# Performance work log

Measured on AMD Instinct MI355X. Metric: run time of the kernel, lower is better.

The kernel has to match this reference:

```python
import jax, jax.numpy as jnp
import numpy as np

P = 8  # patch_size
MD = 32  # metric_dim


def setup_inputs() -> dict:
    key = jax.random.key(0)
    ks = jax.random.split(key, 7)
    b, c, H, W = 4, 3, 512, 512
    s = 1.0 / np.sqrt(MD)
    return {
        "x": jax.random.normal(ks[0], (b, c, H, W), dtype=jnp.float32),
        "conv_w": jax.random.normal(ks[1], (MD, c, P, P), dtype=jnp.float32) * (1.0 / np.sqrt(c * P * P)),
        "conv_b": jax.random.normal(ks[2], (MD,), dtype=jnp.float32) * 0.02,
        "proj_w": jax.random.normal(ks[3], (3 * MD, MD), dtype=jnp.float32) * s,
        "proj_b": jax.random.normal(ks[4], (3 * MD,), dtype=jnp.float32) * 0.02,
        "deconv_w": jax.random.normal(ks[5], (MD, 3, P, P), dtype=jnp.float32) * s,
        "deconv_b": jax.random.normal(ks[6], (3,), dtype=jnp.float32) * 0.02,
    }


def reference(x, conv_w, conv_b, proj_w, proj_b, deconv_w, deconv_b):
    b, c, H, W = x.shape
    hh, ww = H // P, W // P
    # patch embed: Conv2d(kernel=stride=P) == block-reshape + einsum
    xp = x.reshape(b, c, hh, P, ww, P)
    tok = jnp.einsum('bchpwq,ocpq->bohw', xp, conv_w) + conv_b[None, :, None, None]
    # 'b c h w -> b (h w) c'
    tok = tok.reshape(b, MD, hh * ww).transpose(0, 2, 1)  # [b, N, MD]
    xs = tok @ proj_w.T + proj_b
    q, k, v = jnp.split(xs, 3, axis=-1)
    # full NxN QK^T with zeroed diagonal
    lp = jnp.einsum('bnd,bmd->bnm', q, k)
    n = lp.shape[-1]
    i = jnp.arange(n)
    lp = lp.at[:, i, i].set(0.0)
    # cos-phase interference, then matmul with V
    inter = jnp.cos((2.0 * jnp.pi) * lp) @ v  # [b, N, MD]
    # 'b (h w) c -> b c h w'
    inter = inter.transpose(0, 2, 1).reshape(b, MD, hh, ww)
    # ConvTranspose2d(kernel=stride=P) == einsum + block-unreshape
    out = jnp.einsum('bihw,iopq->bohpwq', inter, deconv_w).reshape(b, deconv_w.shape[1], H, W)
    out = out + deconv_b[None, :, None, None]
    return out
```

## Files before the change

### kernel.cpp

```cpp
#include <hip/hip_runtime.h>
#include <hip/hip_bf16.h>

#define NTOK   4096
#define NBATCH 4
#define SPLIT  8

typedef short bf16x8 __attribute__((ext_vector_type(8)));
typedef float f32x4  __attribute__((ext_vector_type(4)));

static __device__ inline short f2bf(float x) {
    __hip_bfloat16 h = __float2bfloat16(x);
    return __builtin_bit_cast(short, h);
}
static __device__ inline float bf2f(short s) {
    return __bfloat162float(__builtin_bit_cast(__hip_bfloat16, s));
}
static __device__ inline f32x4 mfma16(bf16x8 a, bf16x8 b, f32x4 c) {
    return __builtin_amdgcn_mfma_f32_16x16x32_bf16(a, b, c, 0, 0, 0);
}

__global__ __launch_bounds__(512) void k_embed(
    const float* __restrict__ x,  const float* __restrict__ cw,
    const float* __restrict__ cb, const float* __restrict__ pw,
    const float* __restrict__ pb,
    short* __restrict__ qh, short* __restrict__ ql,
    short* __restrict__ kh, short* __restrict__ kl,
    float* __restrict__ vv, float* __restrict__ coef)
{
    __shared__ float tok_lds[64][33];
    __shared__ float qk_lds[64][65];
    const int tid  = threadIdx.x;
    const int og   = tid >> 6;
    const int tl   = tid & 63;
    const int bx   = blockIdx.x;
    const int b    = bx >> 6;
    const int hrow = bx & 63;
    const int n    = hrow * 64 + tl;

    float acc[4];
#pragma unroll
    for (int i = 0; i < 4; ++i) acc[i] = cb[og * 4 + i];

    const float* xb = x + (size_t)b * 3 * 512 * 512;
#pragma unroll
    for (int c = 0; c < 3; ++c) {
        float4 xr[16];
#pragma unroll
        for (int p = 0; p < 8; ++p) {
            const float* row = xb + ((size_t)c * 512 + hrow * 8 + p) * 512 + tl * 8;
            xr[p * 2]     = *(const float4*)row;
            xr[p * 2 + 1] = *(const float4*)(row + 4);
        }
#pragma unroll
        for (int oo = 0; oo < 4; ++oo) {
            const float* wrow = cw + ((size_t)(og * 4 + oo) * 3 + c) * 64;
            float s = 0.f;
#pragma unroll
            for (int j = 0; j < 16; ++j) {
                float4 wv = *(const float4*)(wrow + j * 4);
                s += xr[j].x * wv.x + xr[j].y * wv.y + xr[j].z * wv.z + xr[j].w * wv.w;
            }
            acc[oo] += s;
        }
    }
#pragma unroll
    for (int oo = 0; oo < 4; ++oo) tok_lds[tl][og * 4 + oo] = acc[oo];
    __syncthreads();
    float tok[32];
#pragma unroll
    for (int d = 0; d < 32; ++d) tok[d] = tok_lds[tl][d];

    const int toff = (b * NTOK + n) * 32;
    const int nch  = n >> 4, r16n = n & 15;
#pragma unroll
    for (int g2 = 0; g2 < 3; ++g2) {
        int jb = og * 12 + g2 * 4;
        float r[4];
#pragma unroll
        for (int l2 = 0; l2 < 4; ++l2) {
            int j = jb + l2;
            float s = pb[j];
            const float* prow = pw + j * 32;
#pragma unroll
            for (int d4 = 0; d4 < 8; ++d4) {
                float4 wv = *(const float4*)(prow + d4 * 4);
                s += tok[d4 * 4 + 0] * wv.x + tok[d4 * 4 + 1] * wv.y
                   + tok[d4 * 4 + 2] * wv.z + tok[d4 * 4 + 3] * wv.w;
            }
            r[l2] = s;
        }
        if (jb < 64) {
#pragma unroll
            for (int l2 = 0; l2 < 4; ++l2) qk_lds[tl][jb + l2] = r[l2];
            short hs[4], ls2[4];
#pragma unroll
            for (int l2 = 0; l2 < 4; ++l2) {
                hs[l2]  = f2bf(r[l2]);
                ls2[l2] = f2bf(r[l2] - bf2f(hs[l2]));
            }
            int off = (jb < 32) ? jb : (jb - 32);
            short* dh = (jb < 32) ? qh : kh;
            short* dl = (jb < 32) ? ql : kl;
            size_t pa = ((size_t)(b * 256 + nch) * 64 + ((off >> 3) << 4) + r16n) * 8
                        + (off & 7);
            *(short4*)(dh + pa) = make_short4(hs[0], hs[1], hs[2], hs[3]);
            *(short4*)(dl + pa) = make_short4(ls2[0], ls2[1], ls2[2], ls2[3]);
        } else {
            *(float4*)(vv + toff + (jb - 64)) = make_float4(r[0], r[1], r[2], r[3]);
        }
    }
    __syncthreads();
    if (og == 0) {
        float dp = 0.f;
#pragma unroll
        for (int d = 0; d < 32; ++d) dp += qk_lds[tl][d] * qk_lds[tl][32 + d];
        coef[b * NTOK + n] = 1.f - __builtin_amdgcn_cosf(dp - floorf(dp));
    }
}

__global__ __launch_bounds__(256) void k_varr(
    const float* __restrict__ vv, short* __restrict__ varr)
{
    __shared__ short lds[2048];
    const int tid = threadIdx.x;
    const int bx  = blockIdx.x;
    const int b   = bx >> 7, c = bx & 127;
    const float* vb = vv + ((size_t)b * NTOK + c * 32) * 32;

    const int m  = tid >> 3;
    const int d0 = (tid & 7) * 4;
    float4 v4 = *(const float4*)(vb + tid * 4);
    float vd[4] = {v4.x, v4.y, v4.z, v4.w};
#pragma unroll
    for (int l2 = 0; l2 < 4; ++l2) {
        int d = d0 + l2;
        int dt = d >> 4, r16 = d & 15;
        int g, j;
        if (m < 16) { g = m >> 2; j = m & 3; }
        else        { g = (m - 16) >> 2; j = 4 + ((m - 16) & 3); }
        int lane = g * 16 + r16;
        short hv = f2bf(vd[l2]);
        short lv = f2bf(vd[l2] - bf2f(hv));
        lds[dt * 1024 + 0 * 512 + lane * 8 + j] = hv;
        lds[dt * 1024 + 1 * 512 + lane * 8 + j] = lv;
    }
    __syncthreads();
    *(bf16x8*)(varr + ((size_t)b * 128 + c) * 2048 + tid * 8)
        = *(const bf16x8*)(lds + tid * 8);
}

__global__ __launch_bounds__(256, 3) void k_attn(
    const short* __restrict__ qh, const short* __restrict__ ql,
    const short* __restrict__ kh, const short* __restrict__ kl,
    const short* __restrict__ varr, float* __restrict__ part)
{
    __shared__ float st[128][36];
    const int t = threadIdx.x, l = t & 63, w = t >> 6;
    const int g = l >> 4, r16 = l & 15;
    const int bx = blockIdx.x;
    const int s = bx & 7, b = (bx >> 3) & 3, nb = bx >> 5;
    const int n0 = nb * 128 + w * 32;

    bf16x8 qfh[2], qfl[2];
#pragma unroll
    for (int nt = 0; nt < 2; ++nt) {
        size_t ro = ((size_t)(b * 256 + (n0 >> 4) + nt) * 64 + l) * 8;
        qfh[nt] = *(const bf16x8*)(qh + ro);
        qfl[nt] = *(const bf16x8*)(ql + ro);
    }
    f32x4 acc[2][2];
#pragma unroll
    for (int nt = 0; nt < 2; ++nt)
#pragma unroll
        for (int dt = 0; dt < 2; ++dt)
            acc[nt][dt] = (f32x4){0.f, 0.f, 0.f, 0.f};

    for (int ch = 0; ch < 16; ++ch) {
        const int mc = s * 512 + ch * 32;
        bf16x8 kfh[2], kfl[2];
#pragma unroll
        for (int mh = 0; mh < 2; ++mh) {
            size_t ro = ((size_t)(b * 256 + (mc >> 4) + mh) * 64 + l) * 8;
            kfh[mh] = *(const bf16x8*)(kh + ro);
            kfl[mh] = *(const bf16x8*)(kl + ro);
        }
        const short* vbase = varr + ((size_t)(b * 128 + (mc >> 5))) * 2048;
        bf16x8 vf00 = *(const bf16x8*)(vbase + l * 8);
        bf16x8 vf01 = *(const bf16x8*)(vbase + 512 + l * 8);
        bf16x8 vf10 = *(const bf16x8*)(vbase + 1024 + l * 8);
        bf16x8 vf11 = *(const bf16x8*)(vbase + 1536 + l * 8);

        bf16x8 pah[2], pal[2];
#pragma unroll
        for (int nt = 0; nt < 2; ++nt) {
            f32x4 sa = (f32x4){0.f, 0.f, 0.f, 0.f};
            f32x4 sb = (f32x4){0.f, 0.f, 0.f, 0.f};
            sa = mfma16(kfh[0], qfh[nt], sa);
            sa = mfma16(kfh[0], qfl[nt], sa);
            sa = mfma16(kfl[0], qfh[nt], sa);
            sb = mfma16(kfh[1], qfh[nt], sb);
            sb = mfma16(kfh[1], qfl[nt], sb);
            sb = mfma16(kfl[1], qfh[nt], sb);
#pragma unroll
            for (int r = 0; r < 4; ++r) {
                float xa = sa[r];
                float ca = __builtin_amdgcn_cosf(xa - floorf(xa));
                short ha = f2bf(ca);
                pah[nt][r] = ha;
                pal[nt][r] = f2bf(ca - bf2f(ha));
                float xb2 = sb[r];
                float cb2 = __builtin_amdgcn_cosf(xb2 - floorf(xb2));
                short hb = f2bf(cb2);
                pah[nt][r + 4] = hb;
                pal[nt][r + 4] = f2bf(cb2 - bf2f(hb));
            }
        }
#pragma unroll
        for (int nt = 0; nt < 2; ++nt) {
            acc[nt][0] = mfma16(pah[nt], vf00, acc[nt][0]);
            acc[nt][0] = mfma16(pah[nt], vf01, acc[nt][0]);
            acc[nt][0] = mfma16(pal[nt], vf00, acc[nt][0]);
            acc[nt][1] = mfma16(pah[nt], vf10, acc[nt][1]);
            acc[nt][1] = mfma16(pah[nt], vf11, acc[nt][1]);
            acc[nt][1] = mfma16(pal[nt], vf10, acc[nt][1]);
        }
    }
#pragma unroll
    for (int nt = 0; nt < 2; ++nt)
#pragma unroll
        for (int dt = 0; dt < 2; ++dt)
#pragma unroll
            for (int r = 0; r < 4; ++r)
                st[w * 32 + nt * 16 + 4 * g + r][dt * 16 + r16] = acc[nt][dt][r];
    __syncthreads();
    const int tk = t >> 1, d0 = (t & 1) * 16;
    float* pbp = part + ((size_t)(s * NBATCH + b) * NTOK + nb * 128 + tk) * 32 + d0;
    const float* sp = &st[tk][d0];
#pragma unroll
    for (int q4 = 0; q4 < 4; ++q4)
        *(float4*)(pbp + q4 * 4) = *(const float4*)(sp + q4 * 4);
}

__global__ __launch_bounds__(256) void k_reduce(
    const float* __restrict__ part, const float* __restrict__ vv,
    const float* __restrict__ coef, float* __restrict__ inter)
{
    const int idx = blockIdx.x * 256 + threadIdx.x;
    const int g = idx >> 3, d4 = idx & 7;
    const float* p0 = part + (size_t)g * 32 + d4 * 4;
    float4 s = make_float4(0.f, 0.f, 0.f, 0.f);
#pragma unroll
    for (int sp = 0; sp < SPLIT; ++sp) {
        float4 t = *(const float4*)(p0 + (size_t)sp * (NBATCH * NTOK * 32));
        s.x += t.x; s.y += t.y; s.z += t.z; s.w += t.w;
    }
    const float cf = coef[g];
    float4 v4 = *(const float4*)(vv + (size_t)g * 32 + d4 * 4);
    s.x += cf * v4.x; s.y += cf * v4.y; s.z += cf * v4.z; s.w += cf * v4.w;
    *(float4*)(inter + (size_t)g * 32 + d4 * 4) = s;
}

__global__ __launch_bounds__(512) void k_deconv(
    const float* __restrict__ inter, const float* __restrict__ dw,
    const float* __restrict__ db, float* __restrict__ out)
{
    const int tid  = threadIdx.x;
    const int wv   = tid >> 6;
    const int lane = tid & 63;
    const int bx   = blockIdx.x;
    const int b    = bx >> 6;
    const int hrow = bx & 63;
    const int n    = hrow * 64 + lane;

    float ir[32];
    const float* ip = inter + ((size_t)(b * NTOK + n)) * 32;
#pragma unroll
    for (int d4 = 0; d4 < 8; ++d4) {
        float4 t4 = *(const float4*)(ip + d4 * 4);
        ir[d4 * 4 + 0] = t4.x; ir[d4 * 4 + 1] = t4.y;
        ir[d4 * 4 + 2] = t4.z; ir[d4 * 4 + 3] = t4.w;
    }
#pragma unroll
    for (int rr = 0; rr < 3; ++rr) {
        const int rho = wv * 3 + rr;
        const int o = rho >> 3, p = rho & 7;
        const float bv = db[o];
        float a8[8];
#pragma unroll
        for (int q = 0; q < 8; ++q) a8[q] = bv;
        const float* wbase = dw + o * 64 + p * 8;
#pragma unroll
        for (int i = 0; i < 32; ++i) {
            float4 w0 = *(const float4*)(wbase + (size_t)i * 192);
            float4 w1 = *(const float4*)(wbase + (size_t)i * 192 + 4);
            const float iv = ir[i];
            a8[0] += iv * w0.x; a8[1] += iv * w0.y;
            a8[2] += iv * w0.z; a8[3] += iv * w0.w;
            a8[4] += iv * w1.x; a8[5] += iv * w1.y;
            a8[6] += iv * w1.z; a8[7] += iv * w1.w;
        }
        float* op = out + (((size_t)(b * 3 + o) * 512) + hrow * 8 + p) * 512 + lane * 8;
        *(float4*)op       = make_float4(a8[0], a8[1], a8[2], a8[3]);
        *(float4*)(op + 4) = make_float4(a8[4], a8[5], a8[6], a8[7]);
    }
}

extern "C" void kernel_launch(void* const* d_in, const int* in_sizes, int n_in,
                              void* d_out, int out_size, void* d_ws, size_t ws_size,
                              hipStream_t stream)
{
    const float* x  = (const float*)d_in[0];
    const float* cw = (const float*)d_in[1];
    const float* cb = (const float*)d_in[2];
    const float* pw = (const float*)d_in[3];
    const float* pb = (const float*)d_in[4];
    const float* dw = (const float*)d_in[5];
    const float* db = (const float*)d_in[6];
    float* out = (float*)d_out;

    char* wsb = (char*)d_ws;
    const size_t MB = 1u << 20;
    short* qh    = (short*)(wsb + 0 * MB);
    short* ql    = (short*)(wsb + 1 * MB);
    short* kh    = (short*)(wsb + 2 * MB);
    short* kl    = (short*)(wsb + 3 * MB);
    float* vv    = (float*)(wsb + 4 * MB);
    short* varr  = (short*)(wsb + 6 * MB);
    float* part  = (float*)(wsb + 8 * MB);
    float* coef  = (float*)(wsb + 24 * MB);
    float* inter = (float*)(wsb + 25 * MB);

    hipLaunchKernelGGL(k_embed, dim3(256), dim3(512), 0, stream,
                       x, cw, cb, pw, pb, qh, ql, kh, kl, vv, coef);
    hipLaunchKernelGGL(k_varr, dim3(512), dim3(256), 0, stream, vv, varr);
    hipLaunchKernelGGL(k_attn, dim3(1024), dim3(256), 0, stream,
                       qh, ql, kh, kl, varr, part);
    hipLaunchKernelGGL(k_reduce, dim3(512), dim3(256), 0, stream,
                       part, vv, coef, inter);
    hipLaunchKernelGGL(k_deconv, dim3(256), dim3(512), 0, stream,
                       inter, dw, db, out);
}
```

Measured before the change: 148.5 us.

## Fuse V packing into embed, reduce into deconv, drop low-part of P

```diff
diff --git a/kernel.cpp b/kernel.cpp
--- a/kernel.cpp
+++ b/kernel.cpp
@@ -19,16 +19,18 @@
     return __builtin_amdgcn_mfma_f32_16x16x32_bf16(a, b, c, 0, 0, 0);
 }
 
-__global__ __launch_bounds__(512) void k_embed(
+__global__ __launch_bounds__(256) void k_embed(
     const float* __restrict__ x,  const float* __restrict__ cw,
     const float* __restrict__ cb, const float* __restrict__ pw,
     const float* __restrict__ pb,
     short* __restrict__ qh, short* __restrict__ ql,
     short* __restrict__ kh, short* __restrict__ kl,
-    float* __restrict__ vv, float* __restrict__ coef)
+    float* __restrict__ vv, float* __restrict__ coef,
+    short* __restrict__ varr)
 {
     __shared__ float tok_lds[64][33];
     __shared__ float qk_lds[64][65];
+    __shared__ float v_lds[64][33];
     const int tid  = threadIdx.x;
     const int og   = tid >> 6;
     const int tl   = tid & 63;
@@ -37,9 +39,9 @@
     const int hrow = bx & 63;
     const int n    = hrow * 64 + tl;
 
-    float acc[4];
-#pragma unroll
-    for (int i = 0; i < 4; ++i) acc[i] = cb[og * 4 + i];
+    float acc[8];
+#pragma unroll
+    for (int i = 0; i < 8; ++i) acc[i] = cb[og * 8 + i];
 
     const float* xb = x + (size_t)b * 3 * 512 * 512;
 #pragma unroll
@@ -52,8 +54,8 @@
             xr[p * 2 + 1] = *(const float4*)(row + 4);
         }
 #pragma unroll
-        for (int oo = 0; oo < 4; ++oo) {
-            const float* wrow = cw + ((size_t)(og * 4 + oo) * 3 + c) * 64;
+        for (int oo = 0; oo < 8; ++oo) {
+            const float* wrow = cw + ((size_t)(og * 8 + oo) * 3 + c) * 64;
             float s = 0.f;
 #pragma unroll
             for (int j = 0; j < 16; ++j) {
@@ -64,7 +66,7 @@
         }
     }
 #pragma unroll
-    for (int oo = 0; oo < 4; ++oo) tok_lds[tl][og * 4 + oo] = acc[oo];
+    for (int oo = 0; oo < 8; ++oo) tok_lds[tl][og * 8 + oo] = acc[oo];
     __syncthreads();
     float tok[32];
 #pragma unroll
@@ -73,8 +75,8 @@
     const int toff = (b * NTOK + n) * 32;
     const int nch  = n >> 4, r16n = n & 15;
 #pragma unroll
-    for (int g2 = 0; g2 < 3; ++g2) {
-        int jb = og * 12 + g2 * 4;
+    for (int g2 = 0; g2 < 6; ++g2) {
+        int jb = og * 24 + g2 * 4;
         float r[4];
 #pragma unroll
         for (int l2 = 0; l2 < 4; ++l2) {
@@ -107,6 +109,8 @@
             *(short4*)(dl + pa) = make_short4(ls2[0], ls2[1], ls2[2], ls2[3]);
         } else {
             *(float4*)(vv + toff + (jb - 64)) = make_float4(r[0], r[1], r[2], r[3]);
+#pragma unroll
+            for (int l2 = 0; l2 < 4; ++l2) v_lds[tl][jb - 64 + l2] = r[l2];
         }
     }
     __syncthreads();
@@ -116,37 +120,26 @@
         for (int d = 0; d < 32; ++d) dp += qk_lds[tl][d] * qk_lds[tl][32 + d];
         coef[b * NTOK + n] = 1.f - __builtin_amdgcn_cosf(dp - floorf(dp));
     }
-}
-
-__global__ __launch_bounds__(256) void k_varr(
-    const float* __restrict__ vv, short* __restrict__ varr)
-{
-    __shared__ short lds[2048];
-    const int tid = threadIdx.x;
-    const int bx  = blockIdx.x;
-    const int b   = bx >> 7, c = bx & 127;
-    const float* vb = vv + ((size_t)b * NTOK + c * 32) * 32;
-
-    const int m  = tid >> 3;
-    const int d0 = (tid & 7) * 4;
-    float4 v4 = *(const float4*)(vb + tid * 4);
-    float vd[4] = {v4.x, v4.y, v4.z, v4.w};
-#pragma unroll
-    for (int l2 = 0; l2 < 4; ++l2) {
-        int d = d0 + l2;
-        int dt = d >> 4, r16 = d & 15;
-        int g, j;
-        if (m < 16) { g = m >> 2; j = m & 3; }
-        else        { g = (m - 16) >> 2; j = 4 + ((m - 16) & 3); }
-        int lane = g * 16 + r16;
-        short hv = f2bf(vd[l2]);
-        short lv = f2bf(vd[l2] - bf2f(hv));
-        lds[dt * 1024 + 0 * 512 + lane * 8 + j] = hv;
-        lds[dt * 1024 + 1 * 512 + lane * 8 + j] = lv;
-    }
-    __syncthreads();
-    *(bf16x8*)(varr + ((size_t)b * 128 + c) * 2048 + tid * 8)
-        = *(const bf16x8*)(lds + tid * 8);
+    {
+        const int c_loc = tid >> 7;
+        const int rr    = tid & 127;
+        size_t vout = ((size_t)b * 128 + hrow * 2 + c_loc) * 2048;
+#pragma unroll
+        for (int gi2 = 0; gi2 < 2; ++gi2) {
+            int gi = rr * 2 + gi2;
+            int dt = gi >> 7, hl = (gi >> 6) & 1, lane = gi & 63;
+            int g = lane >> 4, r16 = lane & 15;
+            bf16x8 outv;
+#pragma unroll
+            for (int j = 0; j < 8; ++j) {
+                int m = (j < 4) ? (4 * g + j) : (16 + 4 * g + (j - 4));
+                float xv = v_lds[c_loc * 32 + m][dt * 16 + r16];
+                short hv = f2bf(xv);
+                outv[j] = (hl == 0) ? hv : f2bf(xv - bf2f(hv));
+            }
+            *(bf16x8*)(varr + vout + (size_t)dt * 1024 + hl * 512 + lane * 8) = outv;
+        }
+    }
 }
 
 __global__ __launch_bounds__(256, 3) void k_attn(
@@ -190,7 +183,7 @@
         bf16x8 vf10 = *(const bf16x8*)(vbase + 1024 + l * 8);
         bf16x8 vf11 = *(const bf16x8*)(vbase + 1536 + l * 8);
 
-        bf16x8 pah[2], pal[2];
+        bf16x8 pah[2];
 #pragma unroll
         for (int nt = 0; nt < 2; ++nt) {
             f32x4 sa = (f32x4){0.f, 0.f, 0.f, 0.f};
@@ -204,25 +197,17 @@
 #pragma unroll
             for (int r = 0; r < 4; ++r) {
                 float xa = sa[r];
-                float ca = __builtin_amdgcn_cosf(xa - floorf(xa));
-                short ha = f2bf(ca);
-                pah[nt][r] = ha;
-                pal[nt][r] = f2bf(ca - bf2f(ha));
+                pah[nt][r] = f2bf(__builtin_amdgcn_cosf(xa - floorf(xa)));
                 float xb2 = sb[r];
-                float cb2 = __builtin_amdgcn_cosf(xb2 - floorf(xb2));
-                short hb = f2bf(cb2);
-                pah[nt][r + 4] = hb;
-                pal[nt][r + 4] = f2bf(cb2 - bf2f(hb));
+                pah[nt][r + 4] = f2bf(__builtin_amdgcn_cosf(xb2 - floorf(xb2)));
             }
         }
 #pragma unroll
         for (int nt = 0; nt < 2; ++nt) {
             acc[nt][0] = mfma16(pah[nt], vf00, acc[nt][0]);
             acc[nt][0] = mfma16(pah[nt], vf01, acc[nt][0]);
-            acc[nt][0] = mfma16(pal[nt], vf00, acc[nt][0]);
             acc[nt][1] = mfma16(pah[nt], vf10, acc[nt][1]);
             acc[nt][1] = mfma16(pah[nt], vf11, acc[nt][1]);
-            acc[nt][1] = mfma16(pal[nt], vf10, acc[nt][1]);
         }
     }
 #pragma unroll
@@ -241,45 +226,40 @@
         *(float4*)(pbp + q4 * 4) = *(const float4*)(sp + q4 * 4);
 }
 
-__global__ __launch_bounds__(256) void k_reduce(
+__global__ __launch_bounds__(512) void k_deconv(
     const float* __restrict__ part, const float* __restrict__ vv,
-    const float* __restrict__ coef, float* __restrict__ inter)
-{
-    const int idx = blockIdx.x * 256 + threadIdx.x;
-    const int g = idx >> 3, d4 = idx & 7;
-    const float* p0 = part + (size_t)g * 32 + d4 * 4;
-    float4 s = make_float4(0.f, 0.f, 0.f, 0.f);
-#pragma unroll
-    for (int sp = 0; sp < SPLIT; ++sp) {
-        float4 t = *(const float4*)(p0 + (size_t)sp * (NBATCH * NTOK * 32));
-        s.x += t.x; s.y += t.y; s.z += t.z; s.w += t.w;
-    }
-    const float cf = coef[g];
-    float4 v4 = *(const float4*)(vv + (size_t)g * 32 + d4 * 4);
-    s.x += cf * v4.x; s.y += cf * v4.y; s.z += cf * v4.z; s.w += cf * v4.w;
-    *(float4*)(inter + (size_t)g * 32 + d4 * 4) = s;
-}
-
-__global__ __launch_bounds__(512) void k_deconv(
-    const float* __restrict__ inter, const float* __restrict__ dw,
+    const float* __restrict__ coef, const float* __restrict__ dw,
     const float* __restrict__ db, float* __restrict__ out)
 {
+    __shared__ float inter_lds[64][33];
     const int tid  = threadIdx.x;
-    const int wv   = tid >> 6;
-    const int lane = tid & 63;
     const int bx   = blockIdx.x;
     const int b    = bx >> 6;
     const int hrow = bx & 63;
-    const int n    = hrow * 64 + lane;
-
+
+    {
+        const int tk = tid >> 3, d4 = tid & 7;
+        const int nn = hrow * 64 + tk;
+        const size_t goff = ((size_t)(b * NTOK + nn)) * 32 + d4 * 4;
+        float4 s = make_float4(0.f, 0.f, 0.f, 0.f);
+#pragma unroll
+        for (int sp = 0; sp < SPLIT; ++sp) {
+            float4 t4 = *(const float4*)(part + (size_t)sp * (NBATCH * NTOK * 32) + goff);
+            s.x += t4.x; s.y += t4.y; s.z += t4.z; s.w += t4.w;
+        }
+        const float cf = coef[b * NTOK + nn];
+        float4 v4 = *(const float4*)(vv + goff);
+        s.x += cf * v4.x; s.y += cf * v4.y; s.z += cf * v4.z; s.w += cf * v4.w;
+        inter_lds[tk][d4 * 4 + 0] = s.x; inter_lds[tk][d4 * 4 + 1] = s.y;
+        inter_lds[tk][d4 * 4 + 2] = s.z; inter_lds[tk][d4 * 4 + 3] = s.w;
+    }
+    __syncthreads();
+
+    const int wv   = tid >> 6;
+    const int lane = tid & 63;
     float ir[32];
-    const float* ip = inter + ((size_t)(b * NTOK + n)) * 32;
-#pragma unroll
-    for (int d4 = 0; d4 < 8; ++d4) {
-        float4 t4 = *(const float4*)(ip + d4 * 4);
-        ir[d4 * 4 + 0] = t4.x; ir[d4 * 4 + 1] = t4.y;
-        ir[d4 * 4 + 2] = t4.z; ir[d4 * 4 + 3] = t4.w;
-    }
+#pragma unroll
+    for (int d = 0; d < 32; ++d) ir[d] = inter_lds[lane][d];
 #pragma unroll
     for (int rr = 0; rr < 3; ++rr) {
         const int rho = wv * 3 + rr;
@@ -328,15 +308,11 @@
     short* varr  = (short*)(wsb + 6 * MB);
     float* part  = (float*)(wsb + 8 * MB);
     float* coef  = (float*)(wsb + 24 * MB);
-    float* inter = (float*)(wsb + 25 * MB);
-
-    hipLaunchKernelGGL(k_embed, dim3(256), dim3(512), 0, stream,
-                       x, cw, cb, pw, pb, qh, ql, kh, kl, vv, coef);
-    hipLaunchKernelGGL(k_varr, dim3(512), dim3(256), 0, stream, vv, varr);
+
+    hipLaunchKernelGGL(k_embed, dim3(256), dim3(256), 0, stream,
+                       x, cw, cb, pw, pb, qh, ql, kh, kl, vv, coef, varr);
     hipLaunchKernelGGL(k_attn, dim3(1024), dim3(256), 0, stream,
                        qh, ql, kh, kl, varr, part);
-    hipLaunchKernelGGL(k_reduce, dim3(512), dim3(256), 0, stream,
-                       part, vv, coef, inter);
     hipLaunchKernelGGL(k_deconv, dim3(256), dim3(512), 0, stream,
-                       inter, dw, db, out);
-}
+                       part, vv, coef, dw, db, out);
+}
```

Measured after the change: 143.9 us. 1.03x faster.
